# Performance work log

Hardware: AMD Instinct MI355X
Metric: run time of the kernel (lower is better)

## Reference

```python
import jax, jax.numpy as jnp
import numpy as np

B, N, K, DIM, NB, RES, PAD = 2, 8192, 16, 64, 5, 64, 0.1
H = DIM // 2  # bottleneck width of FKABlock
PLANES = ((0, 1), (0, 2), (1, 2))  # xy, xz, yz


def setup_inputs() -> dict:
    key = jax.random.key(0)
    ks = jax.random.split(key, 10)
    xyz = jax.random.uniform(ks[0], (B, N, 3), jnp.float32) - 0.5

    def w(k, shape, fan_in):
        return jax.random.normal(k, shape, jnp.float32) / np.sqrt(fan_in)

    return {
        "xyz": xyz,
        "w_stem": w(ks[1], (3, DIM), 3),
        "b_stem": jnp.zeros((DIM,), jnp.float32),
        "w0": w(ks[2], (NB, DIM, H), DIM),
        "b0": jnp.zeros((NB, H), jnp.float32),
        "fc1": w(ks[3], (NB, 3, K), 3),
        "fc2": w(ks[4], (NB, 2 * K, K), 2 * K),
        "fc3": w(ks[5], (NB, 2 * K, K), 2 * K),
        "wcv": w(ks[6], (NB, H, H, K), H * K),
        "alpha": jnp.ones((NB,), jnp.float32),
        "beta": jnp.ones((NB,), jnp.float32),
        "w2": w(ks[7], (NB, H, DIM), H),
        "b2": jnp.zeros((NB, DIM), jnp.float32),
    }


def _knn_idx(xyz, k):
    # brute-force squared distances (b, n, n); top-k smallest -> neighbor indices
    sq = jnp.sum(xyz * xyz, -1)
    d2 = sq[:, :, None] + sq[:, None, :] - 2.0 * jnp.einsum('bnd,bmd->bnm', xyz, xyz)
    _, idx = jax.lax.top_k(-d2, k)
    return idx  # (b, n, k) int32


_gather = jax.vmap(lambda f, i: f[i])  # (n, c), (n, k) -> (n, k, c), vmapped over batch


def _fkaconv(x, xyz, idx, fc1, fc2, fc3, wcv, alpha, beta):
    nb_pos = _gather(xyz, idx)                 # (b, n, k, 3)
    pts = nb_pos - xyz[:, :, None, :]          # local coordinates
    # distances are detached in the original (pts.detach())
    dists = jnp.sqrt(jnp.sum(jax.lax.stop_gradient(pts) ** 2, -1) + 1e-12)  # (b, n, k)
    dw = jax.nn.sigmoid(-alpha * dists + beta)
    dw = dw / (jnp.sum(dw, -1, keepdims=True) + 1e-6) * K
    dwe = dw[..., None]                        # (b, n, k, 1)
    # kernel-weight estimation MLP with masked max-pool over neighbors
    m = jax.nn.relu(pts @ fc1)                 # (b, n, k, K)
    mp = jnp.max(m * dwe, 2, keepdims=True)
    m = jax.nn.relu(jnp.concatenate([m, jnp.broadcast_to(mp, m.shape)], -1) @ fc2)
    mp = jnp.max(m * dwe, 2, keepdims=True)
    m = jax.nn.relu(jnp.concatenate([m, jnp.broadcast_to(mp, m.shape)], -1) @ fc3)
    m = m * dwe                                # (b, n, k, K)
    nb_x = _gather(x, idx)                     # (b, n, k, h)
    # f[b,n,c,s] = sum_k nb_x * m ; out[b,n,o] = sum_{c,s} f * wcv[o,c,s]
    return jnp.einsum('bnkc,bnks,ocs->bno', nb_x, m, wcv)


def _triplane(c, xyz):
    pn = xyz / (1.0 + PAD + 1e-3) + 0.5        # normalize to [0, 1]
    ij = jnp.clip((pn * RES).astype(jnp.int32), 0, RES - 1)  # (b, n, 3)
    bidx = jnp.arange(B, dtype=jnp.int32)[:, None]
    cf = c.reshape(B * N, DIM)
    ones = jnp.ones((B * N,), c.dtype)
    planes = []
    for a, b2 in PLANES:
        seg = (bidx * (RES * RES) + ij[..., a] * RES + ij[..., b2]).reshape(-1)
        s = jax.ops.segment_sum(cf, seg, num_segments=B * RES * RES)
        cnt = jax.ops.segment_sum(ones, seg, num_segments=B * RES * RES)
        planes.append((s / jnp.maximum(cnt, 1.0)[:, None]).reshape(B, RES, RES, DIM))
    return jnp.stack(planes, 1)                # (b, 3, res, res, dim)


def reference(xyz, w_stem, b_stem, w0, b0, fc1, fc2, fc3, wcv, alpha, beta, w2, b2):
    c = xyz @ w_stem + b_stem                  # stem linear
    idx = _knn_idx(xyz, K)                     # knn_points(xyz, xyz, K)
    for i in range(NB):                        # FKABlock residual blocks
        x = jax.nn.relu(c @ w0[i] + b0[i])
        x = jax.nn.relu(_fkaconv(x, xyz, idx, fc1[i], fc2[i], fc3[i], wcv[i], alpha[i], beta[i]))
        x = x @ w2[i] + b2[i]
        c = jax.nn.relu(x + c)
    tri_feat = _triplane(c, xyz)
    return (xyz, c, tri_feat)
```

## Files before the change

### kernel.cpp

```cpp
#include <hip/hip_runtime.h>
#include <math.h>

#define BB 2
#define NN 8192
#define KK 16
#define DIMM 64
#define HH 32
#define NBB 5
#define RESS 64
#define NPTS (BB*NN)
#define PLANE_ELEMS (BB*3*RESS*RESS*DIMM)
#define PLANE_CELLS (BB*3*RESS*RESS)
#define GC 8
#define GCS 0.125f
#define NCELL (GC*GC*GC)
#define CAP 640

__global__ void zero_kernel(float* __restrict__ p, int n) {
  int t = blockIdx.x * blockDim.x + threadIdx.x;
  if (t < n) p[t] = 0.0f;
}

__global__ void stem_kernel(const float* __restrict__ xyz,
                            const float* __restrict__ w,
                            const float* __restrict__ bias,
                            float* __restrict__ out_xyz,
                            float* __restrict__ c) {
  int tid = blockIdx.x * blockDim.x + threadIdx.x;
  if (tid < NPTS*3) out_xyz[tid] = xyz[tid];
  if (tid < NPTS*DIMM) {
    int p = tid >> 6, d = tid & 63;
    float x = xyz[p*3+0], y = xyz[p*3+1], z = xyz[p*3+2];
    c[tid] = x*w[d] + y*w[64+d] + z*w[128+d] + bias[d];
  }
}

__device__ __forceinline__ unsigned ord32(float f) {
  unsigned u = __float_as_uint(f);
  return u ^ ((unsigned)((int)u >> 31) | 0x80000000u);
}
__device__ __forceinline__ int cell_of(float v) {
  return min(max((int)((v + 0.5f) * 8.0f), 0), 7);
}

__global__ void knn_count_kernel(const float* __restrict__ xyz,
                                 int* __restrict__ cellcnt) {
  int p = blockIdx.x * blockDim.x + threadIdx.x;
  if (p >= NPTS) return;
  int bq = p >> 13;
  float px = xyz[p*3], py = xyz[p*3+1], pz = xyz[p*3+2];
  int cc = (cell_of(px) << 6) | (cell_of(py) << 3) | cell_of(pz);
  atomicAdd(&cellcnt[(bq << 9) | cc], 1);
}

__global__ __launch_bounds__(1024) void knn_scan_kernel(const int* __restrict__ cnt,
                                                        int* __restrict__ cellstart,
                                                        int* __restrict__ cellcur) {
  __shared__ int s[1024];
  int t = threadIdx.x;
  int v = cnt[t];
  s[t] = v;
  __syncthreads();
  for (int off = 1; off < 1024; off <<= 1) {
    int add = (t >= off) ? s[t-off] : 0;
    __syncthreads();
    s[t] += add;
    __syncthreads();
  }
  int inc = s[t];
  cellstart[t+1] = inc;
  if (t == 0) cellstart[0] = 0;
  cellcur[t] = inc - v;
}

__global__ void knn_scatter_kernel(const float* __restrict__ xyz,
                                   int* __restrict__ cellcur,
                                   float4* __restrict__ spts) {
  int p = blockIdx.x * blockDim.x + threadIdx.x;
  if (p >= NPTS) return;
  int bq = p >> 13;
  float px = xyz[p*3], py = xyz[p*3+1], pz = xyz[p*3+2];
  int cc = (cell_of(px) << 6) | (cell_of(py) << 3) | cell_of(pz);
  int pos = atomicAdd(&cellcur[(bq << 9) | cc], 1);
  spts[pos] = make_float4(px, py, pz, __int_as_float(p & (NN-1)));
}

#define INS64(key)                                                             \
  {                                                                            \
    unsigned long long _k = (key);                                             \
    _Pragma("unroll")                                                          \
    for (int jj = 15; jj >= 1; --jj) {                                         \
      unsigned long long up = bd[jj-1];                                        \
      bool shift = _k < up;                                                    \
      bool here  = _k < bd[jj];                                                \
      unsigned long long nv = shift ? up : _k;                                 \
      bd[jj] = here ? nv : bd[jj];                                             \
    }                                                                          \
    bd[0] = (_k < bd[0]) ? _k : bd[0];                                         \
  }

#define TRYKEY(c4)                                                             \
  {                                                                            \
    float sq = (c4).x*(c4).x + (c4).y*(c4).y + (c4).z*(c4).z;                  \
    float d2 = (qs + sq) - 2.0f*(qx*(c4).x + qy*(c4).y + qz*(c4).z);           \
    unsigned du = ord32(d2);                                                   \
    bool hit = valid && du <= hi15;                                            \
    if (__any(hit)) {                                                          \
      unsigned long long key = hit ?                                           \
          (((unsigned long long)du << 32) | (unsigned)__float_as_int((c4).w))  \
          : ~0ull;                                                             \
      INS64(key);                                                              \
      hi15 = (unsigned)(bd[15] >> 32);                                         \
    }                                                                          \
  }

#define MERGE_STEP(MASK)                                                       \
  {                                                                            \
    unsigned long long tmp[16];                                                \
    _Pragma("unroll")                                                          \
    for (int j = 0; j < 16; ++j) tmp[j] = __shfl_xor(bd[j], MASK);             \
    _Pragma("unroll")                                                          \
    for (int j = 0; j < 16; ++j) {                                             \
      unsigned long long _in = tmp[j];                                         \
      bool dup = false;                                                        \
      _Pragma("unroll")                                                        \
      for (int jj = 0; jj < 16; ++jj) dup = dup || (bd[jj] == _in);            \
      INS64(dup ? ~0ull : _in);                                                \
    }                                                                          \
    hi15 = (unsigned)(bd[15] >> 32);                                           \
  }

__global__ __launch_bounds__(64) void knn_query_kernel(
    const float4* __restrict__ spts, const int* __restrict__ cellstart,
    int* __restrict__ idx) {
  __shared__ __align__(16) float4 s_cand[CAP];
  __shared__ int s_ofs[28];
  __shared__ int s_jlo[27];
  int wave = blockIdx.x;
  int b = wave >> 9;
  int cell = wave & 511;
  int cx = cell >> 6, cy = (cell >> 3) & 7, cz = cell & 7;
  int cb = b << 9;
  int qlo = cellstart[cb + cell], qhi = cellstart[cb + cell + 1];
  int nq = qhi - qlo;
  if (nq <= 0) return;
  int lane = threadIdx.x;
  int q = lane & 15, s = lane >> 4;

  int x0 = max(cx-1,0), x1 = min(cx+1,7);
  int y0 = max(cy-1,0), y1 = min(cy+1,7);
  int z0 = max(cz-1,0), z1 = min(cz+1,7);
  int dy = y1-y0+1, dz = z1-z0+1;
  int count = (x1-x0+1)*dy*dz;
  int len = 0, jlo0 = 0;
  if (lane < count) {
    int xx = x0 + lane/(dy*dz);
    int rem = lane % (dy*dz);
    int yy = y0 + rem/dz, zz = z0 + rem % dz;
    int cc = cb + (xx<<6) + (yy<<3) + zz;
    jlo0 = cellstart[cc];
    len = cellstart[cc+1] - jlo0;
  }
  int pre = len;
#pragma unroll
  for (int off = 1; off < 64; off <<= 1) {
    int v = __shfl_up(pre, off);
    if (lane >= off) pre += v;
  }
  if (lane < count) { s_ofs[lane] = pre - len; s_jlo[lane] = jlo0; }
  if (lane == count-1) s_ofs[count] = pre;
  __syncthreads();
  int total = s_ofs[count];
  int tstag = min(total, CAP);

  for (int w = lane; w < tstag; w += 64) {
    int lo2 = 0, hi2 = count-1;
    while (lo2 < hi2) { int mid = (lo2+hi2+1)>>1; if (s_ofs[mid] <= w) lo2 = mid; else hi2 = mid-1; }
    s_cand[w] = spts[s_jlo[lo2] + (w - s_ofs[lo2])];
  }
  __syncthreads();

  const unsigned thru1 = ord32((GCS - 1e-4f)*(GCS - 1e-4f));
  for (int qg = 0; qg < nq; qg += 16) {
    bool valid = (qg + q) < nq;
    float4 qv = spts[qlo + qg + (valid ? q : 0)];
    float qx = qv.x, qy = qv.y, qz = qv.z;
    float qs = qx*qx + qy*qy + qz*qz;
    unsigned long long bd[16];
#pragma unroll
    for (int j = 0; j < 16; ++j) bd[j] = ~0ull;
    unsigned hi15 = 0xFFFFFFFFu;

    int chunk = (tstag + 3) >> 2;
    int jb = s*chunk, je = min(jb+chunk, tstag);
    for (int j = jb; j < je; ++j) {
      float4 c4 = s_cand[j];
      TRYKEY(c4);
    }
    if (total > CAP) {
      for (int i = 0; i < count; ++i) {
        int ofs_i = s_ofs[i], len_i = s_ofs[i+1]-ofs_i;
        int stg = min(max(CAP - ofs_i, 0), len_i);
        int jl = s_jlo[i] + stg, jh = s_jlo[i] + len_i;
        for (int j2 = jl + s; j2 < jh; j2 += 4) {
          float4 c4 = spts[j2];
          TRYKEY(c4);
        }
      }
    }
    MERGE_STEP(16);
    MERGE_STEP(32);
    bool done = !valid || (hi15 < thru1);
    for (int r = 2; r <= 8; ++r) {
      if (!__any(!done)) break;
      int xs0 = max(cx-r,0), xs1 = min(cx+r,7);
      int ys0 = max(cy-r,0), ys1 = min(cy+r,7);
      int zs0 = max(cz-r,0), zs1 = min(cz+r,7);
      int pr = r-1;
      for (int xx = xs0; xx <= xs1; ++xx)
      for (int yy = ys0; yy <= ys1; ++yy)
      for (int zz = zs0; zz <= zs1; ++zz) {
        if (xx >= cx-pr && xx <= cx+pr && yy >= cy-pr && yy <= cy+pr &&
            zz >= cz-pr && zz <= cz+pr) continue;
        int cc2 = cb + (xx<<6) + (yy<<3) + zz;
        int jl = cellstart[cc2], jh = cellstart[cc2+1];
        for (int j2 = jl + s; j2 < jh; j2 += 4) {
          float4 c4 = spts[j2];
          TRYKEY(c4);
        }
      }
      MERGE_STEP(16);
      MERGE_STEP(32);
      float thr2 = (float)r * GCS - 1e-4f;
      done = !valid || (hi15 < ord32(thr2*thr2));
    }
    if (valid && s == 0) {
      int n_self = __float_as_int(qv.w);
      int* op = idx + (((long)b << 13) + n_self) * 16;
#pragma unroll
      for (int j = 0; j < 16; ++j) op[j] = (int)(unsigned)(bd[j] & 0xffffffffu);
    }
  }
}

__global__ void xproj_kernel(const float* __restrict__ c,
                             const float* __restrict__ w0,
                             const float* __restrict__ b0,
                             float* __restrict__ x, int layer) {
  int tid = blockIdx.x * blockDim.x + threadIdx.x;
  if (tid >= NPTS*HH) return;
  int p = tid >> 5, h = tid & 31;
  const float* w = w0 + layer*DIMM*HH;
  const float* cr = c + p*DIMM;
  float acc = b0[layer*HH + h];
#pragma unroll
  for (int d = 0; d < DIMM; ++d) acc += cr[d]*w[d*HH + h];
  x[tid] = fmaxf(acc, 0.0f);
}

#define OFF_W1   0
#define OFF_W2AT 48
#define OFF_W2BT 368
#define OFF_W3AT 688
#define OFF_W3BT 1008
#define OFF_B2   1328
#define OFF_RED  1392
#define OFF_Y    2416
#define OFF_SCR  2544
#define SCR_SZ   1296
#define S_DW 0
#define S_M1 16
#define S_M2 272
#define S_MM 528
#define S_XN 784
#define S_FB 16
#define LDS_TOT (OFF_SCR + 4*SCR_SZ)

__global__ __launch_bounds__(256) void conv_kernel(
    float* __restrict__ c, const float* __restrict__ x,
    const int* __restrict__ idx, const float* __restrict__ xyz,
    const float* __restrict__ fc1, const float* __restrict__ fc2,
    const float* __restrict__ fc3, const float* __restrict__ wcv,
    const float* __restrict__ alpha, const float* __restrict__ beta,
    const float* __restrict__ w2, const float* __restrict__ b2, int layer)
{
  __shared__ __align__(16) float lds[LDS_TOT];
  int t = threadIdx.x;

  const float* fc1l = fc1 + layer*3*KK;
  const float* fc2l = fc2 + layer*2*KK*KK;
  const float* fc3l = fc3 + layer*2*KK*KK;
  const float* wcvl = wcv + layer*HH*HH*KK;
  const float* w2l  = w2  + layer*HH*DIMM;
  const float* b2l  = b2  + layer*DIMM;

  if (t < 48) lds[OFF_W1 + t] = fc1l[t];
  {
    int s = t >> 4, tt = t & 15;
    lds[OFF_W2AT + s*20 + tt] = fc2l[tt*16 + s];
    lds[OFF_W2BT + s*20 + tt] = fc2l[(16+tt)*16 + s];
    lds[OFF_W3AT + s*20 + tt] = fc3l[tt*16 + s];
    lds[OFF_W3BT + s*20 + tt] = fc3l[(16+tt)*16 + s];
  }
  if (t < 64) lds[OFF_B2 + t] = b2l[t];
  __syncthreads();

  int wv = t >> 6, lane = t & 63;
  int p = blockIdx.x*4 + wv;
  int b = p >> 13;
  float* scr = lds + OFF_SCR + wv*SCR_SZ;
  int sI = lane & 15;

  float qxx = xyz[p*3+0], qyy = xyz[p*3+1], qzz = xyz[p*3+2];
  float alv = alpha[layer], bev = beta[layer];
  int jidx = 0; float px = 0, py = 0, pz = 0, sv = 0;
  if (lane < 16) {
    jidx = idx[p*16 + lane];
    const float* nb = xyz + ((long)b*NN + jidx)*3;
    px = nb[0]-qxx; py = nb[1]-qyy; pz = nb[2]-qzz;
    float dd = sqrtf(px*px + py*py + pz*pz + 1e-12f);
    sv = 1.0f/(1.0f + expf(alv*dd - bev));
  }
  float ssum = 0.0f;
#pragma unroll
  for (int k = 0; k < 16; ++k) ssum += __shfl(sv, k);
  if (lane < 16) scr[S_DW + lane] = sv / (ssum + 1e-6f) * 16.0f;
#pragma unroll
  for (int r = 0; r < 2; ++r) {
    int tsk = lane + 64*r;
    int k = tsk >> 3, seg = tsk & 7;
    int jk = __shfl(jidx, k);
    float4 v = *(const float4*)(x + ((long)b*NN + jk)*32 + seg*4);
    *(float4*)&scr[S_XN + k*32 + seg*4] = v;
  }
#pragma unroll
  for (int r = 0; r < 4; ++r) {
    int k = (lane >> 4) + 4*r;
    float pxk = __shfl(px, k), pyk = __shfl(py, k), pzk = __shfl(pz, k);
    float v = pxk*lds[OFF_W1+sI] + pyk*lds[OFF_W1+16+sI] + pzk*lds[OFF_W1+32+sI];
    scr[S_M1 + k*16 + sI] = fmaxf(v, 0.0f);
  }

  {
    float mpv = 0.0f;
#pragma unroll
    for (int k = 0; k < 16; ++k) mpv = fmaxf(mpv, scr[S_M1 + k*16 + sI] * scr[S_DW + k]);
    float qv = 0.0f;
#pragma unroll
    for (int tt = 0; tt < 16; ++tt) qv += __shfl(mpv, tt) * lds[OFF_W2BT + sI*20 + tt];
    float4 wa0 = *(float4*)&lds[OFF_W2AT + sI*20 + 0];
    float4 wa1 = *(float4*)&lds[OFF_W2AT + sI*20 + 4];
    float4 wa2 = *(float4*)&lds[OFF_W2AT + sI*20 + 8];
    float4 wa3 = *(float4*)&lds[OFF_W2AT + sI*20 + 12];
#pragma unroll
    for (int r = 0; r < 4; ++r) {
      int k = (lane >> 4) + 4*r;
      float4 m0 = *(float4*)&scr[S_M1 + k*16 + 0];
      float4 m1_ = *(float4*)&scr[S_M1 + k*16 + 4];
      float4 m2_ = *(float4*)&scr[S_M1 + k*16 + 8];
      float4 m3_ = *(float4*)&scr[S_M1 + k*16 + 12];
      float v = qv;
      v += m0.x*wa0.x; v += m0.y*wa0.y; v += m0.z*wa0.z; v += m0.w*wa0.w;
      v += m1_.x*wa1.x; v += m1_.y*wa1.y; v += m1_.z*wa1.z; v += m1_.w*wa1.w;
      v += m2_.x*wa2.x; v += m2_.y*wa2.y; v += m2_.z*wa2.z; v += m2_.w*wa2.w;
      v += m3_.x*wa3.x; v += m3_.y*wa3.y; v += m3_.z*wa3.z; v += m3_.w*wa3.w;
      scr[S_M2 + k*16 + sI] = fmaxf(v, 0.0f);
    }
  }

  {
    float mpv = 0.0f;
#pragma unroll
    for (int k = 0; k < 16; ++k) mpv = fmaxf(mpv, scr[S_M2 + k*16 + sI] * scr[S_DW + k]);
    float qv = 0.0f;
#pragma unroll
    for (int tt = 0; tt < 16; ++tt) qv += __shfl(mpv, tt) * lds[OFF_W3BT + sI*20 + tt];
    float4 wa0 = *(float4*)&lds[OFF_W3AT + sI*20 + 0];
    float4 wa1 = *(float4*)&lds[OFF_W3AT + sI*20 + 4];
    float4 wa2 = *(float4*)&lds[OFF_W3AT + sI*20 + 8];
    float4 wa3 = *(float4*)&lds[OFF_W3AT + sI*20 + 12];
#pragma unroll
    for (int r = 0; r < 4; ++r) {
      int k = (lane >> 4) + 4*r;
      float4 m0 = *(float4*)&scr[S_M2 + k*16 + 0];
      float4 m1_ = *(float4*)&scr[S_M2 + k*16 + 4];
      float4 m2_ = *(float4*)&scr[S_M2 + k*16 + 8];
      float4 m3_ = *(float4*)&scr[S_M2 + k*16 + 12];
      float v = qv;
      v += m0.x*wa0.x; v += m0.y*wa0.y; v += m0.z*wa0.z; v += m0.w*wa0.w;
      v += m1_.x*wa1.x; v += m1_.y*wa1.y; v += m1_.z*wa1.z; v += m1_.w*wa1.w;
      v += m2_.x*wa2.x; v += m2_.y*wa2.y; v += m2_.z*wa2.z; v += m2_.w*wa2.w;
      v += m3_.x*wa3.x; v += m3_.y*wa3.y; v += m3_.z*wa3.z; v += m3_.w*wa3.w;
      scr[S_MM + k*16 + sI] = fmaxf(v, 0.0f) * scr[S_DW + k];
    }
  }

  {
    int q4 = lane >> 4;
    float fr0=0,fr1=0,fr2=0,fr3=0,fr4=0,fr5=0,fr6=0,fr7=0;
#pragma unroll
    for (int k = 0; k < 16; ++k) {
      float mmv = scr[S_MM + k*16 + sI];
      float4 a  = *(float4*)&scr[S_XN + k*32 + q4*8];
      float4 bb = *(float4*)&scr[S_XN + k*32 + q4*8 + 4];
      fr0 += a.x*mmv;  fr1 += a.y*mmv;  fr2 += a.z*mmv;  fr3 += a.w*mmv;
      fr4 += bb.x*mmv; fr5 += bb.y*mmv; fr6 += bb.z*mmv; fr7 += bb.w*mmv;
    }
    scr[S_FB + (q4*8+0)*16 + sI] = fr0;
    scr[S_FB + (q4*8+1)*16 + sI] = fr1;
    scr[S_FB + (q4*8+2)*16 + sI] = fr2;
    scr[S_FB + (q4*8+3)*16 + sI] = fr3;
    scr[S_FB + (q4*8+4)*16 + sI] = fr4;
    scr[S_FB + (q4*8+5)*16 + sI] = fr5;
    scr[S_FB + (q4*8+6)*16 + sI] = fr6;
    scr[S_FB + (q4*8+7)*16 + sI] = fr7;
  }
  __syncthreads();

  {
    int o = t & 31, seg = t >> 5;
    const float4* wrow = (const float4*)(wcvl + o*512 + seg*64);
    float acc0=0, acc1=0, acc2=0, acc3=0;
#pragma unroll
    for (int j = 0; j < 16; ++j) {
      float4 w4 = wrow[j];
      float4 f0 = *(const float4*)&lds[OFF_SCR + 0*SCR_SZ + S_FB + seg*64 + j*4];
      float4 f1 = *(const float4*)&lds[OFF_SCR + 1*SCR_SZ + S_FB + seg*64 + j*4];
      float4 f2 = *(const float4*)&lds[OFF_SCR + 2*SCR_SZ + S_FB + seg*64 + j*4];
      float4 f3 = *(const float4*)&lds[OFF_SCR + 3*SCR_SZ + S_FB + seg*64 + j*4];
      acc0 += w4.x*f0.x; acc0 += w4.y*f0.y; acc0 += w4.z*f0.z; acc0 += w4.w*f0.w;
      acc1 += w4.x*f1.x; acc1 += w4.y*f1.y; acc1 += w4.z*f1.z; acc1 += w4.w*f1.w;
      acc2 += w4.x*f2.x; acc2 += w4.y*f2.y; acc2 += w4.z*f2.z; acc2 += w4.w*f2.w;
      acc3 += w4.x*f3.x; acc3 += w4.y*f3.y; acc3 += w4.z*f3.z; acc3 += w4.w*f3.w;
    }
    lds[OFF_RED + seg*128 + 0*32 + o] = acc0;
    lds[OFF_RED + seg*128 + 1*32 + o] = acc1;
    lds[OFF_RED + seg*128 + 2*32 + o] = acc2;
    lds[OFF_RED + seg*128 + 3*32 + o] = acc3;
  }
  __syncthreads();

  if (t < 128) {
    int pt = t >> 5, o = t & 31;
    float yv = 0.0f;
#pragma unroll
    for (int seg = 0; seg < 8; ++seg) yv += lds[OFF_RED + seg*128 + pt*32 + o];
    lds[OFF_Y + pt*32 + o] = fmaxf(yv, 0.0f);
  }
  __syncthreads();

  {
    int pt = t >> 6, d = t & 63;
    float zv = lds[OFF_B2 + d];
    const float* w2g = w2l + d;
#pragma unroll
    for (int o = 0; o < 32; ++o) zv += lds[OFF_Y + pt*32 + o] * w2g[o*64];
    int gp = blockIdx.x*4 + pt;
    float cv = c[gp*64 + d];
    c[gp*64 + d] = fmaxf(zv + cv, 0.0f);
  }
}

__global__ void triacc_kernel(const float* __restrict__ c,
                              const float* __restrict__ xyz,
                              float* __restrict__ psum,
                              float* __restrict__ pcnt) {
  int tid = blockIdx.x * blockDim.x + threadIdx.x;
  if (tid >= NPTS*DIMM) return;
  int p = tid >> 6, d = tid & 63;
  int b = p >> 13;
  float p0 = xyz[p*3+0] / 1.101f + 0.5f;
  float p1 = xyz[p*3+1] / 1.101f + 0.5f;
  float p2 = xyz[p*3+2] / 1.101f + 0.5f;
  int i0 = min(max((int)(p0*64.0f), 0), 63);
  int i1 = min(max((int)(p1*64.0f), 0), 63);
  int i2 = min(max((int)(p2*64.0f), 0), 63);
  int cb = b*3*RESS*RESS;
  int c0 = cb + 0*RESS*RESS + i0*RESS + i1;
  int c1 = cb + 1*RESS*RESS + i0*RESS + i2;
  int c2 = cb + 2*RESS*RESS + i1*RESS + i2;
  float v = c[tid];
  atomicAdd(&psum[c0*DIMM + d], v);
  atomicAdd(&psum[c1*DIMM + d], v);
  atomicAdd(&psum[c2*DIMM + d], v);
  if (d == 0) {
    atomicAdd(&pcnt[c0], 1.0f);
    atomicAdd(&pcnt[c1], 1.0f);
    atomicAdd(&pcnt[c2], 1.0f);
  }
}

__global__ void trinorm_kernel(const float* __restrict__ psum,
                               const float* __restrict__ pcnt,
                               float* __restrict__ out) {
  int tid = blockIdx.x * blockDim.x + threadIdx.x;
  if (tid >= PLANE_ELEMS) return;
  float cnt = pcnt[tid >> 6];
  out[tid] = psum[tid] / fmaxf(cnt, 1.0f);
}

extern "C" void kernel_launch(void* const* d_in, const int* in_sizes, int n_in,
                              void* d_out, int out_size, void* d_ws, size_t ws_size,
                              hipStream_t stream) {
  const float* xyz   = (const float*)d_in[0];
  const float* wstem = (const float*)d_in[1];
  const float* bstem = (const float*)d_in[2];
  const float* w0    = (const float*)d_in[3];
  const float* b0    = (const float*)d_in[4];
  const float* fc1   = (const float*)d_in[5];
  const float* fc2   = (const float*)d_in[6];
  const float* fc3   = (const float*)d_in[7];
  const float* wcv   = (const float*)d_in[8];
  const float* alpha = (const float*)d_in[9];
  const float* beta  = (const float*)d_in[10];
  const float* w2    = (const float*)d_in[11];
  const float* b2    = (const float*)d_in[12];

  float* out     = (float*)d_out;
  float* out_xyz = out;
  float* c       = out + NPTS*3;
  float* out_tri = c + NPTS*DIMM;

  float* wsf  = (float*)d_ws;
  int*   idx  = (int*)d_ws;
  float* x    = wsf + NPTS*16;
  float* psum = x + NPTS*HH;
  float* pcnt = psum + PLANE_ELEMS;

  int*    cellcnt   = (int*)psum;
  int*    cellstart = (int*)psum + 1024;
  int*    cellcur   = (int*)psum + 2056;
  float4* spts      = (float4*)(psum + 4096);

  stem_kernel<<<(NPTS*DIMM+255)/256, 256, 0, stream>>>(xyz, wstem, bstem, out_xyz, c);
  zero_kernel<<<4, 256, 0, stream>>>((float*)cellcnt, 1024);
  knn_count_kernel<<<(NPTS+255)/256, 256, 0, stream>>>(xyz, cellcnt);
  knn_scan_kernel<<<1, 1024, 0, stream>>>(cellcnt, cellstart, cellcur);
  knn_scatter_kernel<<<(NPTS+255)/256, 256, 0, stream>>>(xyz, cellcur, spts);
  knn_query_kernel<<<1024, 64, 0, stream>>>(spts, cellstart, idx);
  for (int layer = 0; layer < NBB; ++layer) {
    xproj_kernel<<<(NPTS*HH+255)/256, 256, 0, stream>>>(c, w0, b0, x, layer);
    conv_kernel<<<NPTS/4, 256, 0, stream>>>(c, x, idx, xyz, fc1, fc2, fc3, wcv,
                                            alpha, beta, w2, b2, layer);
  }
  int nz = PLANE_ELEMS + PLANE_CELLS;
  zero_kernel<<<(nz+255)/256, 256, 0, stream>>>(psum, nz);
  triacc_kernel<<<(NPTS*DIMM+255)/256, 256, 0, stream>>>(c, xyz, psum, pcnt);
  trinorm_kernel<<<(PLANE_ELEMS+255)/256, 256, 0, stream>>>(psum, pcnt, out_tri);
}
```

Measured before the change: 611.0 us.

## Stage radius-2 neighborhood in LDS for boundary cells and use branchless inserts

For grid cells on the domain boundary, the KNN query kernel now stages a radius-2 cell neighborhood, up to 1600 candidates, into shared memory instead of radius 1. These cells often fail the early-exit distance test and fall back to slow global-memory ring expansion. The staged-candidate loop also drops the wave-wide __any branch and always runs the sorted insert. The costs are larger LDS use per block, which can lower occupancy, and more candidates scanned per query for boundary cells.

```diff
diff --git a/kernel.cpp b/kernel.cpp
--- a/kernel.cpp
+++ b/kernel.cpp
@@ -14,7 +14,7 @@
 #define GC 8
 #define GCS 0.125f
 #define NCELL (GC*GC*GC)
-#define CAP 640
+#define CAPB 1600
 
 __global__ void zero_kernel(float* __restrict__ p, int n) {
   int t = blockIdx.x * blockDim.x + threadIdx.x;
@@ -97,6 +97,19 @@
       bd[jj] = here ? nv : bd[jj];                                             \
     }                                                                          \
     bd[0] = (_k < bd[0]) ? _k : bd[0];                                         \
+  }
+
+#define TRYKEY_NB(c4)                                                          \
+  {                                                                            \
+    float sq = (c4).x*(c4).x + (c4).y*(c4).y + (c4).z*(c4).z;                  \
+    float d2 = (qs + sq) - 2.0f*(qx*(c4).x + qy*(c4).y + qz*(c4).z);           \
+    unsigned du = ord32(d2);                                                   \
+    bool hit = valid && du <= hi15;                                            \
+    unsigned long long key = hit ?                                             \
+        (((unsigned long long)du << 32) | (unsigned)__float_as_int((c4).w))    \
+        : ~0ull;                                                               \
+    INS64(key);                                                                \
+    hi15 = (unsigned)(bd[15] >> 32);                                           \
   }
 
 #define TRYKEY(c4)                                                             \
@@ -133,9 +146,9 @@
 __global__ __launch_bounds__(64) void knn_query_kernel(
     const float4* __restrict__ spts, const int* __restrict__ cellstart,
     int* __restrict__ idx) {
-  __shared__ __align__(16) float4 s_cand[CAP];
-  __shared__ int s_ofs[28];
-  __shared__ int s_jlo[27];
+  __shared__ __align__(16) float4 s_cand[CAPB];
+  __shared__ int s_ofs[80];
+  __shared__ int s_jlo[80];
   int wave = blockIdx.x;
   int b = wave >> 9;
   int cell = wave & 511;
@@ -147,31 +160,52 @@
   int lane = threadIdx.x;
   int q = lane & 15, s = lane >> 4;
 
-  int x0 = max(cx-1,0), x1 = min(cx+1,7);
-  int y0 = max(cy-1,0), y1 = min(cy+1,7);
-  int z0 = max(cz-1,0), z1 = min(cz+1,7);
-  int dy = y1-y0+1, dz = z1-z0+1;
-  int count = (x1-x0+1)*dy*dz;
-  int len = 0, jlo0 = 0;
+  bool bound = (cx==0)||(cx==7)||(cy==0)||(cy==7)||(cz==0)||(cz==7);
+  int rs = bound ? 2 : 1;
+  int x0 = max(cx-rs,0), x1 = min(cx+rs,7);
+  int y0 = max(cy-rs,0), y1 = min(cy+rs,7);
+  int z0 = max(cz-rs,0), z1 = min(cz+rs,7);
+  int ny = y1-y0+1, nz2 = z1-z0+1;
+  int count = (x1-x0+1)*ny*nz2;
+
+  int lenA = 0, jloA = 0;
   if (lane < count) {
-    int xx = x0 + lane/(dy*dz);
-    int rem = lane % (dy*dz);
-    int yy = y0 + rem/dz, zz = z0 + rem % dz;
+    int xx = x0 + lane/(ny*nz2);
+    int rem = lane % (ny*nz2);
+    int yy = y0 + rem/nz2, zz = z0 + rem % nz2;
     int cc = cb + (xx<<6) + (yy<<3) + zz;
-    jlo0 = cellstart[cc];
-    len = cellstart[cc+1] - jlo0;
-  }
-  int pre = len;
+    jloA = cellstart[cc];
+    lenA = cellstart[cc+1] - jloA;
+  }
+  int iB = lane + 64, lenB = 0, jloB = 0;
+  if (iB < count) {
+    int xx = x0 + iB/(ny*nz2);
+    int rem = iB % (ny*nz2);
+    int yy = y0 + rem/nz2, zz = z0 + rem % nz2;
+    int cc = cb + (xx<<6) + (yy<<3) + zz;
+    jloB = cellstart[cc];
+    lenB = cellstart[cc+1] - jloB;
+  }
+  int preA = lenA;
 #pragma unroll
   for (int off = 1; off < 64; off <<= 1) {
-    int v = __shfl_up(pre, off);
-    if (lane >= off) pre += v;
-  }
-  if (lane < count) { s_ofs[lane] = pre - len; s_jlo[lane] = jlo0; }
-  if (lane == count-1) s_ofs[count] = pre;
-  __syncthreads();
-  int total = s_ofs[count];
-  int tstag = min(total, CAP);
+    int v = __shfl_up(preA, off);
+    if (lane >= off) preA += v;
+  }
+  int totalA = __shfl(preA, 63);
+  int preB = lenB;
+#pragma unroll
+  for (int off = 1; off < 64; off <<= 1) {
+    int v = __shfl_up(preB, off);
+    if (lane >= off) preB += v;
+  }
+  preB += totalA;
+  int total = __shfl(preB, 63);
+  if (lane < count) { s_ofs[lane] = preA - lenA; s_jlo[lane] = jloA; }
+  if (iB < count)   { s_ofs[iB]   = preB - lenB; s_jlo[iB]   = jloB; }
+  if (lane == 0) s_ofs[count] = total;
+  __syncthreads();
+  int tstag = min(total, CAPB);
 
   for (int w = lane; w < tstag; w += 64) {
     int lo2 = 0, hi2 = count-1;
@@ -180,7 +214,8 @@
   }
   __syncthreads();
 
-  const unsigned thru1 = ord32((GCS - 1e-4f)*(GCS - 1e-4f));
+  float thrS = (float)rs * GCS - 1e-4f;
+  const unsigned thruS = ord32(thrS*thrS);
   for (int qg = 0; qg < nq; qg += 16) {
     bool valid = (qg + q) < nq;
     float4 qv = spts[qlo + qg + (valid ? q : 0)];
@@ -195,12 +230,12 @@
     int jb = s*chunk, je = min(jb+chunk, tstag);
     for (int j = jb; j < je; ++j) {
       float4 c4 = s_cand[j];
-      TRYKEY(c4);
-    }
-    if (total > CAP) {
+      TRYKEY_NB(c4);
+    }
+    if (total > CAPB) {
       for (int i = 0; i < count; ++i) {
         int ofs_i = s_ofs[i], len_i = s_ofs[i+1]-ofs_i;
-        int stg = min(max(CAP - ofs_i, 0), len_i);
+        int stg = min(max(CAPB - ofs_i, 0), len_i);
         int jl = s_jlo[i] + stg, jh = s_jlo[i] + len_i;
         for (int j2 = jl + s; j2 < jh; j2 += 4) {
           float4 c4 = spts[j2];
@@ -210,8 +245,8 @@
     }
     MERGE_STEP(16);
     MERGE_STEP(32);
-    bool done = !valid || (hi15 < thru1);
-    for (int r = 2; r <= 8; ++r) {
+    bool done = !valid || (hi15 < thruS);
+    for (int r = rs+1; r <= 8; ++r) {
       if (!__any(!done)) break;
       int xs0 = max(cx-r,0), xs1 = min(cx+r,7);
       int ys0 = max(cy-r,0), ys1 = min(cy+r,7);
```

Measured after the change: 739.2 us. 21.0% more time.

## Split KNN query cells across multiple blocks and batch top-k insertions

Applied to the files above, without the earlier changes.

The KNN query kernel now launches three blocks per grid cell, each handling an interleaved subset of 16-query groups, which raises parallelism for dense cells. Each block still stages the same neighbor candidates into shared memory, so that load work is repeated. The inner candidate scan also buffers up to four hits per lane in a small register array. It drains them into the sorted top-16 list only when some lane fills up, cutting how often the divergent insertion sort runs. This costs extra registers and redundant staging loads.

```diff
diff --git a/kernel.cpp b/kernel.cpp
--- a/kernel.cpp
+++ b/kernel.cpp
@@ -15,6 +15,7 @@
 #define GCS 0.125f
 #define NCELL (GC*GC*GC)
 #define CAP 640
+#define GRP 3
 
 __global__ void zero_kernel(float* __restrict__ p, int n) {
   int t = blockIdx.x * blockDim.x + threadIdx.x;
@@ -97,6 +98,30 @@
       bd[jj] = here ? nv : bd[jj];                                             \
     }                                                                          \
     bd[0] = (_k < bd[0]) ? _k : bd[0];                                         \
+  }
+
+#define DRAIN64()                                                              \
+  {                                                                            \
+    INS64((0 < fcnt) ? fd[0] : ~0ull);                                         \
+    INS64((1 < fcnt) ? fd[1] : ~0ull);                                         \
+    INS64((2 < fcnt) ? fd[2] : ~0ull);                                         \
+    INS64((3 < fcnt) ? fd[3] : ~0ull);                                         \
+    fcnt = 0; hi15 = (unsigned)(bd[15] >> 32);                                 \
+  }
+
+#define TRYKEY_F(c4)                                                           \
+  {                                                                            \
+    float sq = (c4).x*(c4).x + (c4).y*(c4).y + (c4).z*(c4).z;                  \
+    float d2 = (qs + sq) - 2.0f*(qx*(c4).x + qy*(c4).y + qz*(c4).z);           \
+    unsigned du = ord32(d2);                                                   \
+    bool hit = valid && du <= hi15;                                            \
+    unsigned long long key =                                                   \
+        ((unsigned long long)du << 32) | (unsigned)__float_as_int((c4).w);     \
+    _Pragma("unroll")                                                          \
+    for (int j2 = 0; j2 < 4; ++j2)                                             \
+      fd[j2] = (hit && fcnt == j2) ? key : fd[j2];                             \
+    fcnt += hit;                                                               \
+    if (__any(fcnt >= 4)) { DRAIN64(); }                                       \
   }
 
 #define TRYKEY(c4)                                                             \
@@ -136,14 +161,15 @@
   __shared__ __align__(16) float4 s_cand[CAP];
   __shared__ int s_ofs[28];
   __shared__ int s_jlo[27];
-  int wave = blockIdx.x;
+  int wave = blockIdx.x / GRP;
+  int g = blockIdx.x % GRP;
   int b = wave >> 9;
   int cell = wave & 511;
   int cx = cell >> 6, cy = (cell >> 3) & 7, cz = cell & 7;
   int cb = b << 9;
   int qlo = cellstart[cb + cell], qhi = cellstart[cb + cell + 1];
   int nq = qhi - qlo;
-  if (nq <= 0) return;
+  if (nq <= 0 || 16*g >= nq) return;
   int lane = threadIdx.x;
   int q = lane & 15, s = lane >> 4;
 
@@ -181,7 +207,7 @@
   __syncthreads();
 
   const unsigned thru1 = ord32((GCS - 1e-4f)*(GCS - 1e-4f));
-  for (int qg = 0; qg < nq; qg += 16) {
+  for (int qg = 16*g; qg < nq; qg += 16*GRP) {
     bool valid = (qg + q) < nq;
     float4 qv = spts[qlo + qg + (valid ? q : 0)];
     float qx = qv.x, qy = qv.y, qz = qv.z;
@@ -189,14 +215,17 @@
     unsigned long long bd[16];
 #pragma unroll
     for (int j = 0; j < 16; ++j) bd[j] = ~0ull;
+    unsigned long long fd[4] = {0,0,0,0};
+    int fcnt = 0;
     unsigned hi15 = 0xFFFFFFFFu;
 
     int chunk = (tstag + 3) >> 2;
     int jb = s*chunk, je = min(jb+chunk, tstag);
     for (int j = jb; j < je; ++j) {
       float4 c4 = s_cand[j];
-      TRYKEY(c4);
-    }
+      TRYKEY_F(c4);
+    }
+    if (__any(fcnt > 0)) { DRAIN64(); }
     if (total > CAP) {
       for (int i = 0; i < count; ++i) {
         int ofs_i = s_ofs[i], len_i = s_ofs[i+1]-ofs_i;
@@ -537,7 +566,7 @@
   knn_count_kernel<<<(NPTS+255)/256, 256, 0, stream>>>(xyz, cellcnt);
   knn_scan_kernel<<<1, 1024, 0, stream>>>(cellcnt, cellstart, cellcur);
   knn_scatter_kernel<<<(NPTS+255)/256, 256, 0, stream>>>(xyz, cellcur, spts);
-  knn_query_kernel<<<1024, 64, 0, stream>>>(spts, cellstart, idx);
+  knn_query_kernel<<<1024*GRP, 64, 0, stream>>>(spts, cellstart, idx);
   for (int layer = 0; layer < NBB; ++layer) {
     xproj_kernel<<<(NPTS*HH+255)/256, 256, 0, stream>>>(c, w0, b0, x, layer);
     conv_kernel<<<NPTS/4, 256, 0, stream>>>(c, x, idx, xyz, fc1, fc2, fc3, wcv,
```

Measured after the change: 559.9 us. 8.4% less time.
